# Performance work log

Hardware: AMD Instinct MI355X
Metric: run time of the kernel (lower is better)

## Reference

```python
import jax, jax.numpy as jnp
import numpy as np

TOP_K = 2
NORM_P = 1  # moe_normalize_expert_weights


def setup_inputs() -> dict:
    key = jax.random.key(0)
    k1, k2 = jax.random.split(key)
    B, S, H, E = 4, 4096, 4096, 64
    x = jax.random.normal(k1, (B, S, H), dtype=jnp.float32)
    # Linear(H, E, bias=False) weight, torch layout [E, H]
    W = jax.random.normal(k2, (E, H), dtype=jnp.float32) * (1.0 / np.sqrt(H))
    return {"x": x, "W": W}


def reference(x, W):
    H = x.shape[-1]
    xt = x.reshape(-1, H)                      # [T, H]
    logits = jnp.einsum('th,eh->te', xt, W)    # [T, E]
    scores = jax.nn.softmax(logits, axis=-1)   # [T, E]
    expert_weights, expert_indices = jax.lax.top_k(scores, TOP_K)  # [T, K]
    # p=1 norm over the selected weights (values are positive post-softmax)
    norm = jnp.sum(jnp.abs(expert_weights), axis=-1, keepdims=True)
    expert_weights = expert_weights / norm
    return scores, expert_weights, expert_indices
```

## Files before the change

kernel.cpp:

```cpp
#include <hip/hip_runtime.h>
#include <math.h>

#define TOKS  16384
#define HD    4096
#define NE    64
#define MT    32
#define KT    64
#define NTHR  256
#define LST   72
#define NTILE (HD / KT)

typedef unsigned int   u32;
typedef unsigned short u16;
typedef short v8s __attribute__((ext_vector_type(8)));
typedef float v4f __attribute__((ext_vector_type(4)));

__device__ __forceinline__ void split2(float a, float b, u32& hi, u32& lo) {
    u32 ua = __float_as_uint(a), ub = __float_as_uint(b);
    hi = (ub & 0xffff0000u) | (ua >> 16);
    float la = a - __uint_as_float(ua & 0xffff0000u);
    float lb = b - __uint_as_float(ub & 0xffff0000u);
    lo = (__float_as_uint(lb) & 0xffff0000u) | (__float_as_uint(la) >> 16);
}

__global__ __launch_bounds__(256) void wsplit_kernel(const float* __restrict__ W,
                                                     u16* __restrict__ wh, u16* __restrict__ wl) {
    const int gid = blockIdx.x * 256 + threadIdx.x;
    const float4 f = ((const float4*)W)[gid];
    u32 h0, h1, l0, l1;
    split2(f.x, f.y, h0, l0);
    split2(f.z, f.w, h1, l1);
    u32* whp = (u32*)wh; u32* wlp = (u32*)wl;
    whp[gid * 2 + 0] = h0; whp[gid * 2 + 1] = h1;
    wlp[gid * 2 + 0] = l0; wlp[gid * 2 + 1] = l1;
}

__global__ __launch_bounds__(NTHR, 2) void router_kernel(
    const float* __restrict__ x, const u16* __restrict__ wh, const u16* __restrict__ wl,
    float* __restrict__ scores, float* __restrict__ wout, float* __restrict__ iout)
{
    __shared__ u16 Xh[2][MT][LST], Xl[2][MT][LST];
    __shared__ u16 Wh[2][NE][LST], Wl[2][NE][LST];
    __shared__ float Ls[MT][NE + 1];
    __shared__ float Ssum[MT], Smax[MT];

    const int t    = threadIdx.x;
    const int tok0 = blockIdx.x * MT;
    const int srow = t >> 3, sc = t & 7;
    const int wrow = t >> 2, wc = t & 3;
    const int lane = t & 63;
    const int w    = t >> 6;
    const int wt   = w & 1;
    const int weh  = w >> 1;
    const int q    = lane >> 4, r = lane & 15;
    const int arow  = wt * 16 + r;
    const int brow0 = weh * 32 + r;
    const int brow1 = weh * 32 + 16 + r;

    v4f acc0 = {0.f, 0.f, 0.f, 0.f};
    v4f acc1 = {0.f, 0.f, 0.f, 0.f};

    const size_t xbase = (size_t)(tok0 + srow) * HD;
    const size_t wbase = (size_t)wrow * HD;

    float4 xr0, xr1;
    uint4  whr0, whr1, wlr0, wlr1;

#define LOAD_TILE(K0)                                               \
    do {                                                            \
        xr0  = *(const float4*)&x[xbase + (K0) + sc * 4];           \
        xr1  = *(const float4*)&x[xbase + (K0) + 32 + sc * 4];      \
        whr0 = *(const uint4*)&wh[wbase + (K0) + wc * 8];           \
        whr1 = *(const uint4*)&wh[wbase + (K0) + 32 + wc * 8];      \
        wlr0 = *(const uint4*)&wl[wbase + (K0) + wc * 8];           \
        wlr1 = *(const uint4*)&wl[wbase + (K0) + 32 + wc * 8];      \
    } while (0)

#define STORE_TILE(B)                                               \
    do {                                                            \
        u32 h0, h1, l0, l1;                                         \
        split2(xr0.x, xr0.y, h0, l0);                               \
        split2(xr0.z, xr0.w, h1, l1);                               \
        *(uint2*)&Xh[B][srow][sc * 4]      = make_uint2(h0, h1);    \
        *(uint2*)&Xl[B][srow][sc * 4]      = make_uint2(l0, l1);    \
        split2(xr1.x, xr1.y, h0, l0);                               \
        split2(xr1.z, xr1.w, h1, l1);                               \
        *(uint2*)&Xh[B][srow][32 + sc * 4] = make_uint2(h0, h1);    \
        *(uint2*)&Xl[B][srow][32 + sc * 4] = make_uint2(l0, l1);    \
        *(uint4*)&Wh[B][wrow][wc * 8]      = whr0;                  \
        *(uint4*)&Wh[B][wrow][32 + wc * 8] = whr1;                  \
        *(uint4*)&Wl[B][wrow][wc * 8]      = wlr0;                  \
        *(uint4*)&Wl[B][wrow][32 + wc * 8] = wlr1;                  \
    } while (0)

    LOAD_TILE(0);
    STORE_TILE(0);
    __syncthreads();

    for (int tile = 0; tile < NTILE; ++tile) {
        const int buf = tile & 1;
        if (tile + 1 < NTILE) LOAD_TILE((tile + 1) * KT);
#pragma unroll
        for (int c = 0; c < 2; ++c) {
            const int ko = c * 32 + q * 8;
            v8s ah  = *(const v8s*)&Xh[buf][arow][ko];
            v8s al  = *(const v8s*)&Xl[buf][arow][ko];
            v8s bh0 = *(const v8s*)&Wh[buf][brow0][ko];
            v8s bl0 = *(const v8s*)&Wl[buf][brow0][ko];
            v8s bh1 = *(const v8s*)&Wh[buf][brow1][ko];
            v8s bl1 = *(const v8s*)&Wl[buf][brow1][ko];
            acc0 = __builtin_amdgcn_mfma_f32_16x16x32_bf16(ah, bh0, acc0, 0, 0, 0);
            acc0 = __builtin_amdgcn_mfma_f32_16x16x32_bf16(al, bh0, acc0, 0, 0, 0);
            acc0 = __builtin_amdgcn_mfma_f32_16x16x32_bf16(ah, bl0, acc0, 0, 0, 0);
            acc1 = __builtin_amdgcn_mfma_f32_16x16x32_bf16(ah, bh1, acc1, 0, 0, 0);
            acc1 = __builtin_amdgcn_mfma_f32_16x16x32_bf16(al, bh1, acc1, 0, 0, 0);
            acc1 = __builtin_amdgcn_mfma_f32_16x16x32_bf16(ah, bl1, acc1, 0, 0, 0);
        }
        if (tile + 1 < NTILE) STORE_TILE(buf ^ 1);
        __syncthreads();
    }

#pragma unroll
    for (int reg = 0; reg < 4; ++reg) {
        Ls[wt * 16 + q * 4 + reg][weh * 32 + r]      = acc0[reg];
        Ls[wt * 16 + q * 4 + reg][weh * 32 + 16 + r] = acc1[reg];
    }
    __syncthreads();

    if (t < MT) {
        const int tk = t;
        float m = -3.402823466e+38f;
        for (int e = 0; e < NE; ++e) m = fmaxf(m, Ls[tk][e]);
        float s = 0.f;
        float v1 = -1.f, v2 = -1.f;
        int   i1 = 0, i2 = 0;
        for (int e = 0; e < NE; ++e) {
            const float ex = expf(Ls[tk][e] - m);
            s += ex;
            if (ex > v1)      { v2 = v1; i2 = i1; v1 = ex; i1 = e; }
            else if (ex > v2) { v2 = ex; i2 = e; }
        }
        const float s1 = v1 / s, s2 = v2 / s;
        const float ws_ = s1 + s2;
        wout[(size_t)(tok0 + tk) * 2 + 0] = s1 / ws_;
        wout[(size_t)(tok0 + tk) * 2 + 1] = s2 / ws_;
        iout[(size_t)(tok0 + tk) * 2 + 0] = (float)i1;
        iout[(size_t)(tok0 + tk) * 2 + 1] = (float)i2;
        Ssum[tk] = s;
        Smax[tk] = m;
    }
    __syncthreads();

#pragma unroll
    for (int it = 0; it < (MT * NE) / NTHR; ++it) {
        const int f  = it * NTHR + t;
        const int tk = f >> 6, e = f & 63;
        scores[(size_t)(tok0 + tk) * NE + e] = expf(Ls[tk][e] - Smax[tk]) / Ssum[tk];
    }
}

extern "C" void kernel_launch(void* const* d_in, const int* in_sizes, int n_in,
                              void* d_out, int out_size, void* d_ws, size_t ws_size,
                              hipStream_t stream) {
    (void)in_sizes; (void)n_in; (void)out_size; (void)ws_size;
    const float* x = (const float*)d_in[0];
    const float* W = (const float*)d_in[1];
    float* out    = (float*)d_out;
    float* scores = out;
    float* wout   = scores + (size_t)TOKS * NE;
    float* iout   = wout   + (size_t)TOKS * 2;

    u16* wh = (u16*)d_ws;
    u16* wl = wh + (size_t)NE * HD;

    wsplit_kernel<<<dim3(256), dim3(256), 0, stream>>>(W, wh, wl);
    router_kernel<<<dim3(TOKS / MT), dim3(NTHR), 0, stream>>>(x, wh, wl, scores, wout, iout);
}
```

Before: 393.7 us.

## Stage pre-swizzled W tiles via global_load_lds and feed x directly to MFMA

```diff
diff --git a/kernel.cpp b/kernel.cpp
--- a/kernel.cpp
+++ b/kernel.cpp
@@ -7,7 +7,6 @@
 #define MT    32
 #define KT    64
 #define NTHR  256
-#define LST   72
 #define NTILE (HD / KT)
 
 typedef unsigned int   u32;
@@ -24,30 +23,37 @@
 }
 
 __global__ __launch_bounds__(256) void wsplit_kernel(const float* __restrict__ W,
-                                                     u16* __restrict__ wh, u16* __restrict__ wl) {
+                                                     char* __restrict__ wsd) {
     const int gid = blockIdx.x * 256 + threadIdx.x;
     const float4 f = ((const float4*)W)[gid];
+    const int idx = gid << 2;
+    const int e   = idx >> 12;
+    const int col = idx & 4095;
+    const int k   = col >> 6;
+    const int j   = col & 63;
     u32 h0, h1, l0, l1;
     split2(f.x, f.y, h0, l0);
     split2(f.z, f.w, h1, l1);
-    u32* whp = (u32*)wh; u32* wlp = (u32*)wl;
-    whp[gid * 2 + 0] = h0; whp[gid * 2 + 1] = h1;
-    wlp[gid * 2 + 0] = l0; wlp[gid * 2 + 1] = l1;
-}
+    char* base = wsd + ((size_t)k << 14) + (e << 7) + ((j << 1) ^ ((e & 7) << 4));
+    *(uint2*)(base)        = make_uint2(h0, h1);
+    *(uint2*)(base + 8192) = make_uint2(l0, l1);
+}
+
+#define GLDS(G, L)                                                             \
+    __builtin_amdgcn_global_load_lds(                                          \
+        (const __attribute__((address_space(1))) u32*)(G),                     \
+        (__attribute__((address_space(3))) u32*)(L), 16, 0, 0)
 
 __global__ __launch_bounds__(NTHR, 2) void router_kernel(
-    const float* __restrict__ x, const u16* __restrict__ wh, const u16* __restrict__ wl,
+    const float* __restrict__ x, const char* __restrict__ wsd,
     float* __restrict__ scores, float* __restrict__ wout, float* __restrict__ iout)
 {
-    __shared__ u16 Xh[2][MT][LST], Xl[2][MT][LST];
-    __shared__ u16 Wh[2][NE][LST], Wl[2][NE][LST];
+    __shared__ __align__(16) u16 WT[2][8192];
     __shared__ float Ls[MT][NE + 1];
     __shared__ float Ssum[MT], Smax[MT];
 
     const int t    = threadIdx.x;
     const int tok0 = blockIdx.x * MT;
-    const int srow = t >> 3, sc = t & 7;
-    const int wrow = t >> 2, wc = t & 3;
     const int lane = t & 63;
     const int w    = t >> 6;
     const int wt   = w & 1;
@@ -57,66 +63,92 @@
     const int brow0 = weh * 32 + r;
     const int brow1 = weh * 32 + 16 + r;
 
+    const float* xrow = x + (size_t)(tok0 + arow) * HD;
+    const int qe = q * 8;
+
+    const int sw0 = (brow0 & 7) << 4;
+    const int sw1 = (brow1 & 7) << 4;
+    const int ob0h = brow0 * 128, ob0l = 8192 + ob0h;
+    const int ob1h = brow1 * 128, ob1l = 8192 + ob1h;
+    const int q16 = q * 16;
+    const int c00 = ob0h + ((q16)      ^ sw0);
+    const int c01 = ob0h + ((64 + q16) ^ sw0);
+    const int d00 = ob0l + ((q16)      ^ sw0);
+    const int d01 = ob0l + ((64 + q16) ^ sw0);
+    const int c10 = ob1h + ((q16)      ^ sw1);
+    const int c11 = ob1h + ((64 + q16) ^ sw1);
+    const int d10 = ob1l + ((q16)      ^ sw1);
+    const int d11 = ob1l + ((64 + q16) ^ sw1);
+
+    const char* wsl = wsd + w * 4096 + lane * 16;
+
     v4f acc0 = {0.f, 0.f, 0.f, 0.f};
     v4f acc1 = {0.f, 0.f, 0.f, 0.f};
 
-    const size_t xbase = (size_t)(tok0 + srow) * HD;
-    const size_t wbase = (size_t)wrow * HD;
-
-    float4 xr0, xr1;
-    uint4  whr0, whr1, wlr0, wlr1;
-
-#define LOAD_TILE(K0)                                               \
-    do {                                                            \
-        xr0  = *(const float4*)&x[xbase + (K0) + sc * 4];           \
-        xr1  = *(const float4*)&x[xbase + (K0) + 32 + sc * 4];      \
-        whr0 = *(const uint4*)&wh[wbase + (K0) + wc * 8];           \
-        whr1 = *(const uint4*)&wh[wbase + (K0) + 32 + wc * 8];      \
-        wlr0 = *(const uint4*)&wl[wbase + (K0) + wc * 8];           \
-        wlr1 = *(const uint4*)&wl[wbase + (K0) + 32 + wc * 8];      \
+    float4 a0A, a1A, a2A, a3A, a0B, a1B, a2B, a3B;
+
+#define XLOAD(S, T)                                                 \
+    do { const float* xp = xrow + (T) * KT + qe;                    \
+         a0##S = *(const float4*)(xp);                              \
+         a1##S = *(const float4*)(xp + 4);                          \
+         a2##S = *(const float4*)(xp + 32);                         \
+         a3##S = *(const float4*)(xp + 36); } while (0)
+
+#define STAGE_W(T, B)                                               \
+    do { const char* gs = wsl + ((size_t)(T) << 14);                \
+         char* ls = ((char*)&WT[B][0]) + w * 4096;                  \
+         GLDS(gs,        ls);                                       \
+         GLDS(gs + 1024, ls + 1024);                                \
+         GLDS(gs + 2048, ls + 2048);                                \
+         GLDS(gs + 3072, ls + 3072); } while (0)
+
+#define COMPUTE(S, B)                                                            \
+    do {                                                                         \
+        const char* WB = (const char*)&WT[B][0];                                 \
+        union { v8s v; u32 u[4]; } ah, al;                                       \
+        v8s bh0, bl0, bh1, bl1;                                                  \
+                                                                      \
+        split2(a0##S.x, a0##S.y, ah.u[0], al.u[0]);                              \
+        split2(a0##S.z, a0##S.w, ah.u[1], al.u[1]);                              \
+        split2(a1##S.x, a1##S.y, ah.u[2], al.u[2]);                              \
+        split2(a1##S.z, a1##S.w, ah.u[3], al.u[3]);                              \
+        bh0 = *(const v8s*)(WB + c00); bl0 = *(const v8s*)(WB + d00);            \
+        bh1 = *(const v8s*)(WB + c10); bl1 = *(const v8s*)(WB + d10);            \
+        acc0 = __builtin_amdgcn_mfma_f32_16x16x32_bf16(ah.v, bh0, acc0, 0, 0, 0);\
+        acc0 = __builtin_amdgcn_mfma_f32_16x16x32_bf16(al.v, bh0, acc0, 0, 0, 0);\
+        acc0 = __builtin_amdgcn_mfma_f32_16x16x32_bf16(ah.v, bl0, acc0, 0, 0, 0);\
+        acc1 = __builtin_amdgcn_mfma_f32_16x16x32_bf16(ah.v, bh1, acc1, 0, 0, 0);\
+        acc1 = __builtin_amdgcn_mfma_f32_16x16x32_bf16(al.v, bh1, acc1, 0, 0, 0);\
+        acc1 = __builtin_amdgcn_mfma_f32_16x16x32_bf16(ah.v, bl1, acc1, 0, 0, 0);\
+                                                                      \
+        split2(a2##S.x, a2##S.y, ah.u[0], al.u[0]);                              \
+        split2(a2##S.z, a2##S.w, ah.u[1], al.u[1]);                              \
+        split2(a3##S.x, a3##S.y, ah.u[2], al.u[2]);                              \
+        split2(a3##S.z, a3##S.w, ah.u[3], al.u[3]);                              \
+        bh0 = *(const v8s*)(WB + c01); bl0 = *(const v8s*)(WB + d01);            \
+        bh1 = *(const v8s*)(WB + c11); bl1 = *(const v8s*)(WB + d11);            \
+        acc0 = __builtin_amdgcn_mfma_f32_16x16x32_bf16(ah.v, bh0, acc0, 0, 0, 0);\
+        acc0 = __builtin_amdgcn_mfma_f32_16x16x32_bf16(al.v, bh0, acc0, 0, 0, 0);\
+        acc0 = __builtin_amdgcn_mfma_f32_16x16x32_bf16(ah.v, bl0, acc0, 0, 0, 0);\
+        acc1 = __builtin_amdgcn_mfma_f32_16x16x32_bf16(ah.v, bh1, acc1, 0, 0, 0);\
+        acc1 = __builtin_amdgcn_mfma_f32_16x16x32_bf16(al.v, bh1, acc1, 0, 0, 0);\
+        acc1 = __builtin_amdgcn_mfma_f32_16x16x32_bf16(ah.v, bl1, acc1, 0, 0, 0);\
     } while (0)
 
-#define STORE_TILE(B)                                               \
-    do {                                                            \
-        u32 h0, h1, l0, l1;                                         \
-        split2(xr0.x, xr0.y, h0, l0);                               \
-        split2(xr0.z, xr0.w, h1, l1);                               \
-        *(uint2*)&Xh[B][srow][sc * 4]      = make_uint2(h0, h1);    \
-        *(uint2*)&Xl[B][srow][sc * 4]      = make_uint2(l0, l1);    \
-        split2(xr1.x, xr1.y, h0, l0);                               \
-        split2(xr1.z, xr1.w, h1, l1);                               \
-        *(uint2*)&Xh[B][srow][32 + sc * 4] = make_uint2(h0, h1);    \
-        *(uint2*)&Xl[B][srow][32 + sc * 4] = make_uint2(l0, l1);    \
-        *(uint4*)&Wh[B][wrow][wc * 8]      = whr0;                  \
-        *(uint4*)&Wh[B][wrow][32 + wc * 8] = whr1;                  \
-        *(uint4*)&Wl[B][wrow][wc * 8]      = wlr0;                  \
-        *(uint4*)&Wl[B][wrow][32 + wc * 8] = wlr1;                  \
-    } while (0)
-
-    LOAD_TILE(0);
-    STORE_TILE(0);
+    XLOAD(A, 0);
+    STAGE_W(0, 0);
     __syncthreads();
 
-    for (int tile = 0; tile < NTILE; ++tile) {
-        const int buf = tile & 1;
-        if (tile + 1 < NTILE) LOAD_TILE((tile + 1) * KT);
-#pragma unroll
-        for (int c = 0; c < 2; ++c) {
-            const int ko = c * 32 + q * 8;
-            v8s ah  = *(const v8s*)&Xh[buf][arow][ko];
-            v8s al  = *(const v8s*)&Xl[buf][arow][ko];
-            v8s bh0 = *(const v8s*)&Wh[buf][brow0][ko];
-            v8s bl0 = *(const v8s*)&Wl[buf][brow0][ko];
-            v8s bh1 = *(const v8s*)&Wh[buf][brow1][ko];
-            v8s bl1 = *(const v8s*)&Wl[buf][brow1][ko];
-            acc0 = __builtin_amdgcn_mfma_f32_16x16x32_bf16(ah, bh0, acc0, 0, 0, 0);
-            acc0 = __builtin_amdgcn_mfma_f32_16x16x32_bf16(al, bh0, acc0, 0, 0, 0);
-            acc0 = __builtin_amdgcn_mfma_f32_16x16x32_bf16(ah, bl0, acc0, 0, 0, 0);
-            acc1 = __builtin_amdgcn_mfma_f32_16x16x32_bf16(ah, bh1, acc1, 0, 0, 0);
-            acc1 = __builtin_amdgcn_mfma_f32_16x16x32_bf16(al, bh1, acc1, 0, 0, 0);
-            acc1 = __builtin_amdgcn_mfma_f32_16x16x32_bf16(ah, bl1, acc1, 0, 0, 0);
-        }
-        if (tile + 1 < NTILE) STORE_TILE(buf ^ 1);
+    for (int tt = 0; tt < NTILE; tt += 2) {
+        STAGE_W(tt + 1, 1);
+        XLOAD(B, tt + 1);
+        COMPUTE(A, 0);
+        __syncthreads();
+        if (tt + 2 < NTILE) {
+            STAGE_W(tt + 2, 0);
+            XLOAD(A, tt + 2);
+        }
+        COMPUTE(B, 1);
         __syncthreads();
     }
 
@@ -127,27 +159,50 @@
     }
     __syncthreads();
 
-    if (t < MT) {
-        const int tk = t;
+    {
+        const int tk = t >> 3;
+        const int sl = t & 7;
         float m = -3.402823466e+38f;
-        for (int e = 0; e < NE; ++e) m = fmaxf(m, Ls[tk][e]);
-        float s = 0.f;
-        float v1 = -1.f, v2 = -1.f;
+#pragma unroll
+        for (int j = 0; j < 8; ++j) m = fmaxf(m, Ls[tk][sl + 8 * j]);
+#pragma unroll
+        for (int d = 1; d < 8; d <<= 1) m = fmaxf(m, __shfl_xor(m, d, 64));
+
+        float s = 0.f, v1 = -1.f, v2 = -1.f;
         int   i1 = 0, i2 = 0;
-        for (int e = 0; e < NE; ++e) {
+#pragma unroll
+        for (int j = 0; j < 8; ++j) {
+            const int e = sl + 8 * j;
             const float ex = expf(Ls[tk][e] - m);
             s += ex;
             if (ex > v1)      { v2 = v1; i2 = i1; v1 = ex; i1 = e; }
             else if (ex > v2) { v2 = ex; i2 = e; }
         }
-        const float s1 = v1 / s, s2 = v2 / s;
-        const float ws_ = s1 + s2;
-        wout[(size_t)(tok0 + tk) * 2 + 0] = s1 / ws_;
-        wout[(size_t)(tok0 + tk) * 2 + 1] = s2 / ws_;
-        iout[(size_t)(tok0 + tk) * 2 + 0] = (float)i1;
-        iout[(size_t)(tok0 + tk) * 2 + 1] = (float)i2;
-        Ssum[tk] = s;
-        Smax[tk] = m;
+#pragma unroll
+        for (int d = 1; d < 8; d <<= 1) {
+            const float ov1 = __shfl_xor(v1, d, 64);
+            const int   oi1 = __shfl_xor(i1, d, 64);
+            const float ov2 = __shfl_xor(v2, d, 64);
+            const int   oi2 = __shfl_xor(i2, d, 64);
+            s += __shfl_xor(s, d, 64);
+            if (ov1 > v1 || (ov1 == v1 && oi1 < i1)) {
+                if (ov2 > v1 || (ov2 == v1 && oi2 < i1)) { v2 = ov2; i2 = oi2; }
+                else                                     { v2 = v1;  i2 = i1;  }
+                v1 = ov1; i1 = oi1;
+            } else if (ov1 > v2 || (ov1 == v2 && oi1 < i2)) {
+                v2 = ov1; i2 = oi1;
+            }
+        }
+        if (sl == 0) {
+            const float s1 = v1 / s, s2 = v2 / s;
+            const float ws_ = s1 + s2;
+            wout[(size_t)(tok0 + tk) * 2 + 0] = s1 / ws_;
+            wout[(size_t)(tok0 + tk) * 2 + 1] = s2 / ws_;
+            iout[(size_t)(tok0 + tk) * 2 + 0] = (float)i1;
+            iout[(size_t)(tok0 + tk) * 2 + 1] = (float)i2;
+            Ssum[tk] = s;
+            Smax[tk] = m;
+        }
     }
     __syncthreads();
 
@@ -170,9 +225,8 @@
     float* wout   = scores + (size_t)TOKS * NE;
     float* iout   = wout   + (size_t)TOKS * 2;
 
-    u16* wh = (u16*)d_ws;
-    u16* wl = wh + (size_t)NE * HD;
-
-    wsplit_kernel<<<dim3(256), dim3(256), 0, stream>>>(W, wh, wl);
-    router_kernel<<<dim3(TOKS / MT), dim3(NTHR), 0, stream>>>(x, wh, wl, scores, wout, iout);
-}
+    char* wsd = (char*)d_ws;
+
+    wsplit_kernel<<<dim3(256), dim3(256), 0, stream>>>(W, wsd);
+    router_kernel<<<dim3(TOKS / MT), dim3(NTHR), 0, stream>>>(x, wsd, scores, wout, iout);
+}
```

Result: no change. 398.2 us (+1.2%).
